# Kernel optimization log

Hardware: AMD Instinct MI355X
Metric: run time of the kernel (lower is better)

The kernel has to match this reference:

```python
import jax, jax.numpy as jnp
import numpy as np

E = 1_000_000      # number of edges
N_NODE = 200_000   # nodes in this layer's frontier
IN_DIM = 64
ATTN_DIM = 64
OUT_DIM = 64
N_REL = 200
N_ENT = 50_000
B = 8              # batchsize


def setup_inputs() -> dict:
    key = jax.random.key(0)
    ks = jax.random.split(key, 16)
    # edges columns: [r_idx, _, rel, _, sub, obj]
    r_idx = jax.random.randint(ks[0], (E,), 0, B)
    rel = jax.random.randint(ks[1], (E,), 0, 2 * N_REL + 1)
    sub = jax.random.randint(ks[2], (E,), 0, N_NODE)
    obj = jax.random.randint(ks[3], (E,), 0, N_NODE)
    zeros = jnp.zeros((E,), dtype=jnp.int64 if jax.config.jax_enable_x64 else jnp.int32)
    edges = jnp.stack([r_idx, zeros, rel, zeros, sub, obj], axis=1)

    q_sub = jax.random.randint(ks[4], (B,), 0, N_ENT)
    q_rel = jax.random.randint(ks[5], (B,), 0, 2 * N_REL + 1)
    hidden = jax.random.normal(ks[6], (N_NODE, IN_DIM), dtype=jnp.float32)
    nodes = jnp.stack([jax.random.randint(ks[7], (N_NODE,), 0, B),
                       jax.random.randint(ks[8], (N_NODE,), 0, N_ENT)], axis=1)
    old_nodes_new_idx = jnp.sort(jax.random.randint(ks[9], (N_NODE // 2,), 0, N_NODE))

    s = 1.0 / np.sqrt(IN_DIM)
    rela_embed = jax.random.normal(ks[10], (2 * N_REL + 1, IN_DIM), dtype=jnp.float32)
    Ws = jax.random.uniform(ks[11], (ATTN_DIM, IN_DIM), minval=-s, maxval=s)  # Ws_attn.weight
    Wr = jax.random.uniform(ks[12], (ATTN_DIM, IN_DIM), minval=-s, maxval=s)  # Wr_attn.weight
    Wqr_W = jax.random.uniform(ks[13], (ATTN_DIM, IN_DIM), minval=-s, maxval=s)
    Wqr_b = jax.random.uniform(ks[14], (ATTN_DIM,), minval=-s, maxval=s)
    sa = 1.0 / np.sqrt(ATTN_DIM)
    kk = jax.random.split(ks[15], 3)
    wa_W = jax.random.uniform(kk[0], (1, ATTN_DIM), minval=-sa, maxval=sa)  # w_alpha.weight
    wa_b = jax.random.uniform(kk[1], (1,), minval=-sa, maxval=sa)
    Wh = jax.random.uniform(kk[2], (OUT_DIM, IN_DIM), minval=-s, maxval=s)  # W_h.weight

    return {"q_sub": q_sub, "q_rel": q_rel, "hidden": hidden, "edges": edges,
            "nodes": nodes, "old_nodes_new_idx": old_nodes_new_idx, "batchsize": B,
            "rela_embed": rela_embed, "Ws": Ws, "Wr": Wr, "Wqr_W": Wqr_W,
            "Wqr_b": Wqr_b, "wa_W": wa_W, "wa_b": wa_b, "Wh": Wh}


def reference(q_sub, q_rel, hidden, edges, nodes, old_nodes_new_idx, batchsize,
              rela_embed, Ws, Wr, Wqr_W, Wqr_b, wa_W, wa_b, Wh):
    sub = edges[:, 4]
    rel = edges[:, 2]
    obj = edges[:, 5]
    r_idx = edges[:, 0]
    n_node = nodes.shape[0]

    hs = hidden[sub]                      # [E, in_dim] gather
    hr = rela_embed[rel]                  # [E, in_dim]
    h_qr = rela_embed[q_rel][r_idx]       # [E, in_dim]

    # attention MLP: relu(Ws hs + Wr hr + Wqr h_qr + b) -> scalar -> sigmoid gate
    attn_input = (jnp.einsum('ei,ai->ea', hs, Ws)
                  + jnp.einsum('ei,ai->ea', hr, Wr)
                  + jnp.einsum('ei,ai->ea', h_qr, Wqr_W) + Wqr_b)  # [E, attn_dim]
    alpha = jax.nn.sigmoid(jax.nn.relu(attn_input) @ wa_W.T + wa_b)  # [E, 1]

    message = alpha * (hs + hr)                                       # [E, in_dim]
    message_agg = jax.ops.segment_sum(message, obj, num_segments=n_node)  # [n_node, in_dim]
    hidden_new = message_agg @ Wh.T  # act is identity (default)
    return hidden_new
```

## Files before the change

### kernel.cpp

```cpp
#include <hip/hip_runtime.h>
#include <hip/hip_bf16.h>


__global__ __launch_bounds__(256) void rowproj64(const float* src,
                                                 const float* __restrict__ W,
                                                 float* dst, int nrows) {
    __shared__ float Wt[64][65];
    __shared__ float4 Sl[64][16];
    int tid = threadIdx.x;
    for (int i = tid; i < 4096; i += 256) Wt[i & 63][i >> 6] = W[i];
    long r0 = (long)blockIdx.x * 64;
    const float4* src4 = (const float4*)(src + r0 * 64);
    float4* s4 = (float4*)Sl;
    for (int i = tid; i < 1024; i += 256) s4[i] = src4[i];
    __syncthreads();
    int c = tid & 63;
    int rbase = (tid >> 6) * 16;
    float w[64];
#pragma unroll
    for (int k = 0; k < 64; ++k) w[k] = Wt[k][c];
#pragma unroll
    for (int r = 0; r < 16; ++r) {
        float a0 = 0.f, a1 = 0.f, a2 = 0.f, a3 = 0.f;
#pragma unroll
        for (int k4 = 0; k4 < 16; ++k4) {
            float4 s = Sl[rbase + r][k4];
            a0 += s.x * w[4 * k4 + 0];
            a1 += s.y * w[4 * k4 + 1];
            a2 += s.z * w[4 * k4 + 2];
            a3 += s.w * w[4 * k4 + 3];
        }
        dst[(r0 + rbase + r) * 64 + c] = (a0 + a1) + (a2 + a3);
    }
}

__global__ void relproj(const float* __restrict__ rela,
                        const float* __restrict__ W,
                        float* __restrict__ out) {
    int r = blockIdx.x, a = threadIdx.x;
    __shared__ float h[64];
    h[a] = rela[r * 64 + a];
    __syncthreads();
    float acc = 0.f;
#pragma unroll
    for (int k = 0; k < 64; ++k) acc += h[k] * W[a * 64 + k];
    out[r * 64 + a] = acc;
}

__global__ void qrproj(const float* __restrict__ rela,
                       const int* __restrict__ q_rel,
                       const float* __restrict__ Wqr,
                       const float* __restrict__ bqr,
                       float* __restrict__ out) {
    int b = blockIdx.x, a = threadIdx.x;
    int qr = q_rel[b];
    __shared__ float h[64];
    h[a] = rela[qr * 64 + a];
    __syncthreads();
    float acc = bqr[a];
#pragma unroll
    for (int k = 0; k < 64; ++k) acc += h[k] * Wqr[a * 64 + k];
    out[b * 64 + a] = acc;
}

__global__ void build_ct(const float* __restrict__ hrproj,
                         const float* __restrict__ hqrproj,
                         float* __restrict__ ct, int n_rel_tot) {
    int idx = blockIdx.x;
    int a = threadIdx.x;
    int b = idx / n_rel_tot, r = idx - b * n_rel_tot;
    ct[(size_t)idx * 64 + a] = hrproj[r * 64 + a] + hqrproj[b * 64 + a];
}

__global__ void k_count(const int* __restrict__ edges, int E,
                        int* __restrict__ deg) {
    int e = blockIdx.x * blockDim.x + threadIdx.x;
    if (e < E) atomicAdd(&deg[edges[(size_t)e * 6 + 5]], 1);
}

#define SCAN_BS 256
__global__ __launch_bounds__(SCAN_BS) void k_scan_block(
    const int* __restrict__ deg, int N,
    int* __restrict__ rowptr, int* __restrict__ bsum) {
    __shared__ int sh[SCAN_BS];
    int t = threadIdx.x, b = blockIdx.x;
    int base = b * 1024 + t * 4;
    int d0 = (base + 0 < N) ? deg[base + 0] : 0;
    int d1 = (base + 1 < N) ? deg[base + 1] : 0;
    int d2 = (base + 2 < N) ? deg[base + 2] : 0;
    int d3 = (base + 3 < N) ? deg[base + 3] : 0;
    int s = d0 + d1 + d2 + d3;
    sh[t] = s;
    __syncthreads();
    for (int o = 1; o < SCAN_BS; o <<= 1) {
        int v = (t >= o) ? sh[t - o] : 0;
        __syncthreads();
        sh[t] += v;
        __syncthreads();
    }
    int run = sh[t] - s;
    if (t == SCAN_BS - 1) bsum[b] = sh[t];
    if (base + 0 < N) rowptr[base + 0] = run;  run += d0;
    if (base + 1 < N) rowptr[base + 1] = run;  run += d1;
    if (base + 2 < N) rowptr[base + 2] = run;  run += d2;
    if (base + 3 < N) rowptr[base + 3] = run;
}

__global__ __launch_bounds__(SCAN_BS) void k_scan_partials(
    const int* __restrict__ bsum, int* __restrict__ boffs, int NB) {
    __shared__ int sh[SCAN_BS];
    int t = threadIdx.x;
    int v = (t < NB) ? bsum[t] : 0;
    sh[t] = v;
    __syncthreads();
    for (int o = 1; o < SCAN_BS; o <<= 1) {
        int u = (t >= o) ? sh[t - o] : 0;
        __syncthreads();
        sh[t] += u;
        __syncthreads();
    }
    if (t < NB) boffs[t] = sh[t] - v;
}

__global__ void k_add_offsets(int* __restrict__ rowptr,
                              int* __restrict__ cursor,
                              const int* __restrict__ boffs, int N, int E) {
    int i = blockIdx.x * blockDim.x + threadIdx.x;
    if (i < N) {
        int v = rowptr[i] + boffs[i >> 10];
        rowptr[i] = v;
        cursor[i] = v;
    }
    if (i == 0) rowptr[N] = E;
}

__global__ __launch_bounds__(256) void k_scatter(
    const int* __restrict__ edges, int E,
    const float* __restrict__ hproj,
    const float* __restrict__ ct, int n_rel_tot,
    const float* __restrict__ wa,
    const float* __restrict__ wab_p,
    int* __restrict__ cursor,
    unsigned int* __restrict__ key,
    float* __restrict__ aval) {
    int lane = threadIdx.x & 63;
    int half = lane >> 5;
    int li   = lane & 31;
    int wid = __builtin_amdgcn_readfirstlane(
        (int)((blockIdx.x * blockDim.x + threadIdx.x) >> 6));
    int nw = (int)((gridDim.x * blockDim.x) >> 6);
    int npairs = (E + 1) >> 1;
    int per = (npairs + nw - 1) / nw;
    int p0 = wid * per;
    int p1 = min(p0 + per, npairs);

    const float2* hproj2 = (const float2*)hproj;
    const float2* ct2    = (const float2*)ct;
    float2 wav = ((const float2*)wa)[li];
    float wab = wab_p[0];

    for (int p = p0; p < p1; ++p) {
        int e0 = 2 * p, e1 = e0 + 1;
        bool v1 = e1 < E;
        const int* ed0 = edges + (size_t)e0 * 6;
        const int* ed1 = edges + (size_t)(v1 ? e1 : e0) * 6;
        int r_idx = half ? ed1[0] : ed0[0];
        int rel   = half ? ed1[2] : ed0[2];
        int sub   = half ? ed1[4] : ed0[4];
        int obj   = half ? ed1[5] : ed0[5];

        size_t sb = (size_t)sub * 32 + li;
        float2 hp = hproj2[sb];
        float2 cv = ct2[((size_t)r_idx * n_rel_tot + rel) * 32 + li];
        float t = fmaxf(hp.x + cv.x, 0.f) * wav.x
                + fmaxf(hp.y + cv.y, 0.f) * wav.y;
#pragma unroll
        for (int o = 16; o; o >>= 1) t += __shfl_xor(t, o, 64);
        float alpha = 1.f / (1.f + __expf(-(t + wab)));

        if (li == 0 && (!half || v1)) {
            int pos = atomicAdd(&cursor[obj], 1);
            key[pos] = (unsigned int)sub | ((unsigned int)rel << 18);
            aval[pos] = alpha;
        }
    }
}

__global__ __launch_bounds__(256) void k_aggregate(
    const int* __restrict__ rowptr,
    const unsigned int* __restrict__ key,
    const float* __restrict__ aval,
    const float* __restrict__ hidden,
    const float* __restrict__ rela,
    float* __restrict__ agg, int N) {
    int lane = threadIdx.x & 63;
    int w = (int)((blockIdx.x * blockDim.x + threadIdx.x) >> 6);
    if (w >= N) return;
    int n = __builtin_amdgcn_readfirstlane(w);
    int s = rowptr[n], e = rowptr[n + 1];
    float acc = 0.f;
    if (s < e) {
        unsigned int k = key[s];
        float a = aval[s];
        for (int j = s + 1; j < e; ++j) {
            unsigned int kn = key[j];
            float an = aval[j];
            int sub = (int)(k & 0x3FFFFu);
            int rel = (int)(k >> 18);
            acc += a * (hidden[(size_t)sub * 64 + lane] + rela[rel * 64 + lane]);
            k = kn;
            a = an;
        }
        int sub = (int)(k & 0x3FFFFu);
        int rel = (int)(k >> 18);
        acc += a * (hidden[(size_t)sub * 64 + lane] + rela[rel * 64 + lane]);
    }
    agg[(size_t)n * 64 + lane] = acc;
}

extern "C" void kernel_launch(void* const* d_in, const int* in_sizes, int n_in,
                              void* d_out, int out_size, void* d_ws, size_t ws_size,
                              hipStream_t stream) {
    const int* q_rel    = (const int*)d_in[1];
    const float* hidden = (const float*)d_in[2];
    const int* edges    = (const int*)d_in[3];
    const float* rela   = (const float*)d_in[7];
    const float* Ws     = (const float*)d_in[8];
    const float* Wr     = (const float*)d_in[9];
    const float* WqrW   = (const float*)d_in[10];
    const float* Wqrb   = (const float*)d_in[11];
    const float* waW    = (const float*)d_in[12];
    const float* wab    = (const float*)d_in[13];
    const float* Wh     = (const float*)d_in[14];

    int E = in_sizes[3] / 6;
    int n_node = in_sizes[4] / 2;
    int n_rel_tot = in_sizes[7] / 64;
    int B = in_sizes[0];
    int NB = (n_node + 1023) / 1024;

    float* agg = (float*)d_out;
    char* w = (char*)d_ws;
    float* hproj   = (float*)w;                w += (size_t)n_node * 64 * 4;
    float* hrproj  = (float*)w;                w += (size_t)n_rel_tot * 64 * 4;
    float* hqrproj = (float*)w;                w += (size_t)B * 64 * 4;
    float* ct      = (float*)w;                w += (size_t)B * n_rel_tot * 64 * 4;
    float* aval    = (float*)w;                w += (size_t)E * 4;
    unsigned int* key = (unsigned int*)w;      w += (size_t)E * 4;
    int* deg    = (int*)w;                     w += (size_t)n_node * 4;
    int* cursor = (int*)w;                     w += (size_t)n_node * 4;
    int* rowptr = (int*)w;                     w += (size_t)(n_node + 1) * 4;
    int* bsum   = (int*)w;                     w += (size_t)NB * 4;
    int* boffs  = (int*)w;                     w += (size_t)NB * 4;

    rowproj64<<<n_node / 64, 256, 0, stream>>>(hidden, Ws, hproj, n_node);
    relproj<<<n_rel_tot, 64, 0, stream>>>(rela, Wr, hrproj);
    qrproj<<<B, 64, 0, stream>>>(rela, q_rel, WqrW, Wqrb, hqrproj);
    build_ct<<<B * n_rel_tot, 64, 0, stream>>>(hrproj, hqrproj, ct, n_rel_tot);

    hipMemsetAsync(deg, 0, (size_t)n_node * 4, stream);
    k_count<<<(E + 255) / 256, 256, 0, stream>>>(edges, E, deg);
    k_scan_block<<<NB, SCAN_BS, 0, stream>>>(deg, n_node, rowptr, bsum);
    k_scan_partials<<<1, SCAN_BS, 0, stream>>>(bsum, boffs, NB);
    k_add_offsets<<<(n_node + 255) / 256, 256, 0, stream>>>(rowptr, cursor,
                                                            boffs, n_node, E);

    k_scatter<<<2048, 256, 0, stream>>>(edges, E, hproj, ct, n_rel_tot,
                                        waW, wab, cursor, key, aval);
    k_aggregate<<<(n_node * 64 + 255) / 256, 256, 0, stream>>>(
        rowptr, key, aval, hidden, rela, agg, n_node);
    rowproj64<<<n_node / 64, 256, 0, stream>>>(agg, Wh, agg, n_node);
}
```

Before: 458.5 us.

## Fuse attention gate computation into CSR aggregation and merge ct setup kernels

```diff
diff --git a/kernel.cpp b/kernel.cpp
--- a/kernel.cpp
+++ b/kernel.cpp
@@ -34,42 +34,27 @@
     }
 }
 
-__global__ void relproj(const float* __restrict__ rela,
-                        const float* __restrict__ W,
-                        float* __restrict__ out) {
-    int r = blockIdx.x, a = threadIdx.x;
-    __shared__ float h[64];
-    h[a] = rela[r * 64 + a];
-    __syncthreads();
-    float acc = 0.f;
-#pragma unroll
-    for (int k = 0; k < 64; ++k) acc += h[k] * W[a * 64 + k];
-    out[r * 64 + a] = acc;
-}
-
-__global__ void qrproj(const float* __restrict__ rela,
-                       const int* __restrict__ q_rel,
-                       const float* __restrict__ Wqr,
-                       const float* __restrict__ bqr,
-                       float* __restrict__ out) {
-    int b = blockIdx.x, a = threadIdx.x;
-    int qr = q_rel[b];
-    __shared__ float h[64];
-    h[a] = rela[qr * 64 + a];
-    __syncthreads();
-    float acc = bqr[a];
-#pragma unroll
-    for (int k = 0; k < 64; ++k) acc += h[k] * Wqr[a * 64 + k];
-    out[b * 64 + a] = acc;
-}
-
-__global__ void build_ct(const float* __restrict__ hrproj,
-                         const float* __restrict__ hqrproj,
-                         float* __restrict__ ct, int n_rel_tot) {
-    int idx = blockIdx.x;
-    int a = threadIdx.x;
-    int b = idx / n_rel_tot, r = idx - b * n_rel_tot;
-    ct[(size_t)idx * 64 + a] = hrproj[r * 64 + a] + hqrproj[b * 64 + a];
+__global__ void k_ct(const float* __restrict__ rela,
+                     const int* __restrict__ q_rel,
+                     const float* __restrict__ Wr,
+                     const float* __restrict__ Wqr,
+                     const float* __restrict__ bqr,
+                     float* __restrict__ ct, int B) {
+    int rel = blockIdx.x, a = threadIdx.x;
+    __shared__ float hr[64];
+    __shared__ float hq[8][64];
+    hr[a] = rela[(size_t)rel * 64 + a];
+    for (int b = 0; b < B; ++b) hq[b][a] = rela[(size_t)q_rel[b] * 64 + a];
+    __syncthreads();
+    float accr = 0.f;
+#pragma unroll
+    for (int k = 0; k < 64; ++k) accr += hr[k] * Wr[a * 64 + k];
+    for (int b = 0; b < B; ++b) {
+        float acc = bqr[a];
+#pragma unroll
+        for (int k = 0; k < 64; ++k) acc += hq[b][k] * Wqr[a * 64 + k];
+        ct[((size_t)rel * 8 + b) * 64 + a] = accr + acc;
+    }
 }
 
 __global__ void k_count(const int* __restrict__ edges, int E,
@@ -134,86 +119,63 @@
     if (i == 0) rowptr[N] = E;
 }
 
-__global__ __launch_bounds__(256) void k_scatter(
-    const int* __restrict__ edges, int E,
+__global__ void k_key(const int* __restrict__ edges, int E,
+                      int* __restrict__ cursor,
+                      unsigned int* __restrict__ key) {
+    int e = blockIdx.x * blockDim.x + threadIdx.x;
+    if (e >= E) return;
+    const int* ed = edges + (size_t)e * 6;
+    int r_idx = ed[0], rel = ed[2], sub = ed[4], obj = ed[5];
+    int pos = atomicAdd(&cursor[obj], 1);
+    key[pos] = (unsigned int)sub | ((unsigned int)(rel * 8 + r_idx) << 18);
+}
+
+__global__ __launch_bounds__(256) void k_agg(
+    const int* __restrict__ rowptr,
+    const unsigned int* __restrict__ key,
     const float* __restrict__ hproj,
-    const float* __restrict__ ct, int n_rel_tot,
+    const float* __restrict__ ct,
+    const float* __restrict__ hidden,
+    const float* __restrict__ rela,
     const float* __restrict__ wa,
     const float* __restrict__ wab_p,
-    int* __restrict__ cursor,
-    unsigned int* __restrict__ key,
-    float* __restrict__ aval) {
-    int lane = threadIdx.x & 63;
-    int half = lane >> 5;
-    int li   = lane & 31;
-    int wid = __builtin_amdgcn_readfirstlane(
-        (int)((blockIdx.x * blockDim.x + threadIdx.x) >> 6));
-    int nw = (int)((gridDim.x * blockDim.x) >> 6);
-    int npairs = (E + 1) >> 1;
-    int per = (npairs + nw - 1) / nw;
-    int p0 = wid * per;
-    int p1 = min(p0 + per, npairs);
-
-    const float2* hproj2 = (const float2*)hproj;
-    const float2* ct2    = (const float2*)ct;
-    float2 wav = ((const float2*)wa)[li];
-    float wab = wab_p[0];
-
-    for (int p = p0; p < p1; ++p) {
-        int e0 = 2 * p, e1 = e0 + 1;
-        bool v1 = e1 < E;
-        const int* ed0 = edges + (size_t)e0 * 6;
-        const int* ed1 = edges + (size_t)(v1 ? e1 : e0) * 6;
-        int r_idx = half ? ed1[0] : ed0[0];
-        int rel   = half ? ed1[2] : ed0[2];
-        int sub   = half ? ed1[4] : ed0[4];
-        int obj   = half ? ed1[5] : ed0[5];
-
-        size_t sb = (size_t)sub * 32 + li;
-        float2 hp = hproj2[sb];
-        float2 cv = ct2[((size_t)r_idx * n_rel_tot + rel) * 32 + li];
-        float t = fmaxf(hp.x + cv.x, 0.f) * wav.x
-                + fmaxf(hp.y + cv.y, 0.f) * wav.y;
-#pragma unroll
-        for (int o = 16; o; o >>= 1) t += __shfl_xor(t, o, 64);
-        float alpha = 1.f / (1.f + __expf(-(t + wab)));
-
-        if (li == 0 && (!half || v1)) {
-            int pos = atomicAdd(&cursor[obj], 1);
-            key[pos] = (unsigned int)sub | ((unsigned int)rel << 18);
-            aval[pos] = alpha;
-        }
-    }
-}
-
-__global__ __launch_bounds__(256) void k_aggregate(
-    const int* __restrict__ rowptr,
-    const unsigned int* __restrict__ key,
-    const float* __restrict__ aval,
-    const float* __restrict__ hidden,
-    const float* __restrict__ rela,
     float* __restrict__ agg, int N) {
     int lane = threadIdx.x & 63;
     int w = (int)((blockIdx.x * blockDim.x + threadIdx.x) >> 6);
     if (w >= N) return;
     int n = __builtin_amdgcn_readfirstlane(w);
     int s = rowptr[n], e = rowptr[n + 1];
+    float wav = wa[lane];
+    float wab = wab_p[0];
     float acc = 0.f;
     if (s < e) {
-        unsigned int k = key[s];
-        float a = aval[s];
+        unsigned int k0 = key[s];
+        int sub = (int)(k0 & 0x3FFFFu);
+        int cr  = (int)(k0 >> 18);
+        float hp = hproj[(size_t)sub * 64 + lane];
+        float cv = ct[(size_t)cr * 64 + lane];
+        float hd = hidden[(size_t)sub * 64 + lane];
+        float rl = rela[(size_t)(cr >> 3) * 64 + lane];
         for (int j = s + 1; j < e; ++j) {
-            unsigned int kn = key[j];
-            float an = aval[j];
-            int sub = (int)(k & 0x3FFFFu);
-            int rel = (int)(k >> 18);
-            acc += a * (hidden[(size_t)sub * 64 + lane] + rela[rel * 64 + lane]);
-            k = kn;
-            a = an;
+            unsigned int k1 = key[j];
+            int sub1 = (int)(k1 & 0x3FFFFu);
+            int cr1  = (int)(k1 >> 18);
+            float hp1 = hproj[(size_t)sub1 * 64 + lane];
+            float cv1 = ct[(size_t)cr1 * 64 + lane];
+            float hd1 = hidden[(size_t)sub1 * 64 + lane];
+            float rl1 = rela[(size_t)(cr1 >> 3) * 64 + lane];
+            float t = fmaxf(hp + cv, 0.f) * wav;
+#pragma unroll
+            for (int o = 32; o; o >>= 1) t += __shfl_xor(t, o, 64);
+            float alpha = 1.f / (1.f + __expf(-(t + wab)));
+            acc += alpha * (hd + rl);
+            hp = hp1; cv = cv1; hd = hd1; rl = rl1;
         }
-        int sub = (int)(k & 0x3FFFFu);
-        int rel = (int)(k >> 18);
-        acc += a * (hidden[(size_t)sub * 64 + lane] + rela[rel * 64 + lane]);
+        float t = fmaxf(hp + cv, 0.f) * wav;
+#pragma unroll
+        for (int o = 32; o; o >>= 1) t += __shfl_xor(t, o, 64);
+        float alpha = 1.f / (1.f + __expf(-(t + wab)));
+        acc += alpha * (hd + rl);
     }
     agg[(size_t)n * 64 + lane] = acc;
 }
@@ -241,11 +203,8 @@
 
     float* agg = (float*)d_out;
     char* w = (char*)d_ws;
-    float* hproj   = (float*)w;                w += (size_t)n_node * 64 * 4;
-    float* hrproj  = (float*)w;                w += (size_t)n_rel_tot * 64 * 4;
-    float* hqrproj = (float*)w;                w += (size_t)B * 64 * 4;
-    float* ct      = (float*)w;                w += (size_t)B * n_rel_tot * 64 * 4;
-    float* aval    = (float*)w;                w += (size_t)E * 4;
+    float* hproj = (float*)w;                  w += (size_t)n_node * 64 * 4;
+    float* ct    = (float*)w;                  w += (size_t)n_rel_tot * 8 * 64 * 4;
     unsigned int* key = (unsigned int*)w;      w += (size_t)E * 4;
     int* deg    = (int*)w;                     w += (size_t)n_node * 4;
     int* cursor = (int*)w;                     w += (size_t)n_node * 4;
@@ -254,9 +213,7 @@
     int* boffs  = (int*)w;                     w += (size_t)NB * 4;
 
     rowproj64<<<n_node / 64, 256, 0, stream>>>(hidden, Ws, hproj, n_node);
-    relproj<<<n_rel_tot, 64, 0, stream>>>(rela, Wr, hrproj);
-    qrproj<<<B, 64, 0, stream>>>(rela, q_rel, WqrW, Wqrb, hqrproj);
-    build_ct<<<B * n_rel_tot, 64, 0, stream>>>(hrproj, hqrproj, ct, n_rel_tot);
+    k_ct<<<n_rel_tot, 64, 0, stream>>>(rela, q_rel, Wr, WqrW, Wqrb, ct, B);
 
     hipMemsetAsync(deg, 0, (size_t)n_node * 4, stream);
     k_count<<<(E + 255) / 256, 256, 0, stream>>>(edges, E, deg);
@@ -265,9 +222,8 @@
     k_add_offsets<<<(n_node + 255) / 256, 256, 0, stream>>>(rowptr, cursor,
                                                             boffs, n_node, E);
 
-    k_scatter<<<2048, 256, 0, stream>>>(edges, E, hproj, ct, n_rel_tot,
-                                        waW, wab, cursor, key, aval);
-    k_aggregate<<<(n_node * 64 + 255) / 256, 256, 0, stream>>>(
-        rowptr, key, aval, hidden, rela, agg, n_node);
+    k_key<<<(E + 255) / 256, 256, 0, stream>>>(edges, E, cursor, key);
+    k_agg<<<(n_node * 64 + 255) / 256, 256, 0, stream>>>(
+        rowptr, key, hproj, ct, hidden, rela, waW, wab, agg, n_node);
     rowproj64<<<n_node / 64, 256, 0, stream>>>(agg, Wh, agg, n_node);
 }
```

After: 448.4 us. 2.2% less time.
